# Kernel tuning notes

Hardware: AMD Instinct MI355X
Metric: run time of the kernel (lower is better)

## Reference

```python
import jax, jax.numpy as jnp
import numpy as np

B, S, E = 4, 2048, 2048
NH, NKV, HD = 16, 4, 128  # num_heads, num_kv_heads, head_dim
GROUP = NH // NKV


def setup_inputs() -> dict:
    key = jax.random.key(0)
    ks = jax.random.split(key, 6)
    sc = 0.02
    return {
        "hidden_states": jax.random.normal(ks[0], (B, S, E), dtype=jnp.float32),
        "q_w": jax.random.normal(ks[1], (E, NH * HD), dtype=jnp.float32) * sc,
        "k_w": jax.random.normal(ks[2], (E, NKV * HD), dtype=jnp.float32) * sc,
        "v_w": jax.random.normal(ks[3], (E, NKV * HD), dtype=jnp.float32) * sc,
        "out_w": jax.random.normal(ks[4], (NH * HD, E), dtype=jnp.float32) * sc,
        "out_b": jnp.zeros((E,), dtype=jnp.float32),
    }


def reference(hidden_states, q_w, k_w, v_w, out_w, out_b):
    x = hidden_states
    # projections (no bias on q/k/v, bias on out_proj)
    q = (x @ q_w).reshape(B, S, NH, HD).transpose(0, 2, 1, 3)    # [B,NH,S,HD]
    k = (x @ k_w).reshape(B, S, NKV, HD).transpose(0, 2, 1, 3)   # [B,NKV,S,HD]
    v = (x @ v_w).reshape(B, S, NKV, HD).transpose(0, 2, 1, 3)   # [B,NKV,S,HD]

    # GQA: each kv head serves GROUP consecutive query heads (matches loop order)
    k_exp = jnp.repeat(k, GROUP, axis=1)  # [B,NH,S,HD]
    v_exp = jnp.repeat(v, GROUP, axis=1)

    # GPT-Neo: fp32 attention, NO 1/sqrt(d) scaling
    qf = q.astype(jnp.float32)
    kf = k_exp.astype(jnp.float32)
    scores = jnp.einsum("bhqd,bhkd->bhqk", qf, kf)  # [B,NH,S,S]

    causal = jnp.tril(jnp.ones((S, S), dtype=bool))[None, None]
    mask_value = jnp.finfo(scores.dtype).min
    scores = jnp.where(causal, scores, mask_value)

    attn = jax.nn.softmax(scores, axis=-1).astype(v.dtype)
    ctx = jnp.einsum("bhqk,bhkd->bhqd", attn, v_exp)  # [B,NH,S,HD]

    out = ctx.transpose(0, 2, 1, 3).reshape(B, S, NH * HD)
    return out @ out_w + out_b
```

## Files before the change

kernel.cpp:

```cpp
#include <hip/hip_runtime.h>

typedef unsigned short u16;
typedef unsigned int   u32;
typedef __attribute__((ext_vector_type(8))) _Float16 f16x8;
typedef __attribute__((ext_vector_type(2))) __fp16   fp16x2;
typedef __attribute__((ext_vector_type(4))) float    f32x4;

#define LOG2E 1.44269504088896340f

__device__ __forceinline__ u16 f2h(float x) {
  union { _Float16 h; u16 u; } c;
  c.h = (_Float16)x;
  return c.u;
}
__device__ __forceinline__ u32 pk2(float a, float b) {
  union { fp16x2 h; u32 u; } c;
  c.h = __builtin_amdgcn_cvt_pkrtz(a, b);
  return c.u;
}
__device__ __forceinline__ void swap32(u32& a, u32& b) {
  asm volatile("v_permlane32_swap_b32 %0, %1" : "+v"(a), "+v"(b));
}
__device__ __forceinline__ void swap16(u32& a, u32& b) {
  asm volatile("v_permlane16_swap_b32 %0, %1" : "+v"(a), "+v"(b));
}
__device__ __forceinline__ void gload16(const u16* g, u16* l) {
  __builtin_amdgcn_global_load_lds(
      (const __attribute__((address_space(1))) void*)g,
      (__attribute__((address_space(3))) void*)l, 16, 0, 0);
}
__device__ __forceinline__ f32x4 MFMA(f16x8 a, f16x8 b, f32x4 c) {
  return __builtin_amdgcn_mfma_f32_16x16x32_f16(a, b, c, 0, 0, 0);
}

__global__ void conv_f16(const float4* __restrict__ src, u16* __restrict__ d, int n4) {
  int i = blockIdx.x * 256 + threadIdx.x;
  if (i >= n4) return;
  float4 v = src[i];
  union { u16 u[4]; uint2 q; } H;
  H.u[0] = f2h(v.x); H.u[1] = f2h(v.y); H.u[2] = f2h(v.z); H.u[3] = f2h(v.w);
  *(uint2*)&d[(size_t)i * 4] = H.q;
}

__global__ void transpose_f16(const float* __restrict__ src, int K, int N,
                              u16* __restrict__ d, int rowOff) {
  __shared__ float t[32][33];
  int n0 = blockIdx.x * 32, k0 = blockIdx.y * 32;
  int tx = threadIdx.x, ty = threadIdx.y;
#pragma unroll
  for (int i = 0; i < 4; ++i)
    t[ty + 8 * i][tx] = src[(size_t)(k0 + ty + 8 * i) * N + n0 + tx];
  __syncthreads();
#pragma unroll
  for (int i = 0; i < 4; ++i) {
    int n = n0 + ty + 8 * i, k = k0 + tx;
    d[(size_t)(rowOff + n) * 2048 + k] = f2h(t[tx][ty + 8 * i]);
  }
}

__global__ __launch_bounds__(512) void gemm_qkv(
    const u16* __restrict__ A, const u16* __restrict__ B,
    u16* __restrict__ Qf, u16* __restrict__ Kf, u16* __restrict__ VT) {
  const int K = 2048;
  const int NS = K / 32;
  __shared__ u16 As[3][256 * 32];
  __shared__ u16 Bs[3][128 * 32];
  int tid = threadIdx.x;
  int l = tid & 63, w = tid >> 6;
  int lr = l & 15, lg = l >> 4;
  int wr = w >> 1, wc = w & 1;
  int r0 = tid >> 2;
  int ssrc = (((tid & 3) ^ ((r0 >> 1) & 3))) * 8;
  size_t half = (size_t)128 * K;
  int swz = (lr >> 1) & 3;
  int aoff = (wr * 64 + lr) * 32 + (lg ^ swz) * 8;
  int boff = (wc * 64 + lr) * 32 + (lg ^ swz) * 8;

  for (int job = blockIdx.x; job < 768; job += 512) {
    int lidx = (job & 7) * 96 + (job >> 3);
    int bx = lidx % 24, by = lidx / 24;
    int rowA = by * 256, colB = bx * 128;
    const u16* ga = A + (size_t)(rowA + r0) * K + ssrc;
    const u16* gb = B + (size_t)(colB + r0) * K + ssrc;
    f32x4 acc[4][4] = {};

    gload16(ga, &As[0][tid * 8]);
    gload16(ga + half, &As[0][4096 + tid * 8]);
    gload16(gb, &Bs[0][tid * 8]);
    gload16(ga + 32, &As[1][tid * 8]);
    gload16(ga + 32 + half, &As[1][4096 + tid * 8]);
    gload16(gb + 32, &Bs[1][tid * 8]);
    asm volatile("s_waitcnt vmcnt(3)" ::: "memory");
    __builtin_amdgcn_sched_barrier(0);
    __builtin_amdgcn_s_barrier();
    __builtin_amdgcn_sched_barrier(0);

    for (int t = 0; t < NS; ++t) {
      int cur = t % 3, nxt = (t + 2) % 3;
      bool pre = (t + 2 < NS);
      int kb2 = (t + 2) * 32;
      f16x8 ah[4], bh[4];
#pragma unroll
      for (int i = 0; i < 4; ++i)
        ah[i] = *(const f16x8*)&As[cur][aoff + i * 512];
#pragma unroll
      for (int j = 0; j < 4; ++j)
        bh[j] = *(const f16x8*)&Bs[cur][boff + j * 512];
      if (pre) {
        gload16(ga + kb2, &As[nxt][tid * 8]);
        gload16(ga + kb2 + half, &As[nxt][4096 + tid * 8]);
        gload16(gb + kb2, &Bs[nxt][tid * 8]);
      }
      __builtin_amdgcn_s_setprio(1);
#pragma unroll
      for (int i = 0; i < 4; ++i)
#pragma unroll
        for (int j = 0; j < 4; ++j)
          acc[i][j] = MFMA(ah[i], bh[j], acc[i][j]);
      __builtin_amdgcn_s_setprio(0);
      if (pre) {
        asm volatile("s_waitcnt vmcnt(3)" ::: "memory");
      } else {
        asm volatile("s_waitcnt vmcnt(0)" ::: "memory");
      }
      __builtin_amdgcn_sched_barrier(0);
      __builtin_amdgcn_s_barrier();
      __builtin_amdgcn_sched_barrier(0);
    }

#pragma unroll
    for (int i = 0; i < 4; ++i) {
      int row0 = rowA + wr * 64 + i * 16 + lg * 4;
#pragma unroll
      for (int j = 0; j < 4; ++j) {
        int c = colB + wc * 64 + j * 16 + lr;
        f32x4 v = acc[i][j];
        if (c < 2048) {
#pragma unroll
          for (int r = 0; r < 4; ++r)
            Qf[(size_t)(row0 + r) * 2048 + c] = f2h(v[r]);
        } else if (c < 2560) {
          int ck = c - 2048;
#pragma unroll
          for (int r = 0; r < 4; ++r)
            Kf[(size_t)(row0 + r) * 512 + ck] = f2h(v[r]);
        } else {
          int cv = c - 2560, kvh = cv >> 7, d = cv & 127;
          int b = row0 >> 11, t2 = row0 & 2047;
          union { u16 u[4]; uint2 q; } P;
#pragma unroll
          for (int r = 0; r < 4; ++r) P.u[r] = f2h(v[r]);
          *(uint2*)&VT[((size_t)(b * 4 + kvh) * 128 + d) * 2048 + t2] = P.q;
        }
      }
    }
    __builtin_amdgcn_s_barrier();
    __builtin_amdgcn_sched_barrier(0);
  }
}

__global__ __launch_bounds__(512) void gemm_out(
    const u16* __restrict__ A, const u16* __restrict__ B,
    float* __restrict__ Out, const float* __restrict__ bias) {
  const int K = 2048;
  const int NS = K / 32;
  __shared__ u16 As[3][256 * 32];
  __shared__ u16 Bs[3][128 * 32];
  int tid = threadIdx.x;
  int l = tid & 63, w = tid >> 6;
  int lr = l & 15, lg = l >> 4;
  int wr = w >> 1, wc = w & 1;
  int p = blockIdx.x;
  int lidx = (p & 7) * 64 + (p >> 3);
  int bx = lidx & 15, by = lidx >> 4;
  int rowA = by * 256, colB = bx * 128;
  int r0 = tid >> 2;
  int ssrc = (((tid & 3) ^ ((r0 >> 1) & 3))) * 8;
  const u16* ga = A + (size_t)(rowA + r0) * K + ssrc;
  const u16* gb = B + (size_t)(colB + r0) * K + ssrc;
  size_t half = (size_t)128 * K;
  f32x4 acc[4][4] = {};
  int swz = (lr >> 1) & 3;
  int aoff = (wr * 64 + lr) * 32 + (lg ^ swz) * 8;
  int boff = (wc * 64 + lr) * 32 + (lg ^ swz) * 8;

  gload16(ga, &As[0][tid * 8]);
  gload16(ga + half, &As[0][4096 + tid * 8]);
  gload16(gb, &Bs[0][tid * 8]);
  gload16(ga + 32, &As[1][tid * 8]);
  gload16(ga + 32 + half, &As[1][4096 + tid * 8]);
  gload16(gb + 32, &Bs[1][tid * 8]);
  asm volatile("s_waitcnt vmcnt(3)" ::: "memory");
  __builtin_amdgcn_sched_barrier(0);
  __builtin_amdgcn_s_barrier();
  __builtin_amdgcn_sched_barrier(0);

  for (int t = 0; t < NS; ++t) {
    int cur = t % 3, nxt = (t + 2) % 3;
    bool pre = (t + 2 < NS);
    int kb2 = (t + 2) * 32;
    f16x8 ah[4], bh[4];
#pragma unroll
    for (int i = 0; i < 4; ++i)
      ah[i] = *(const f16x8*)&As[cur][aoff + i * 512];
#pragma unroll
    for (int j = 0; j < 4; ++j)
      bh[j] = *(const f16x8*)&Bs[cur][boff + j * 512];
    if (pre) {
      gload16(ga + kb2, &As[nxt][tid * 8]);
      gload16(ga + kb2 + half, &As[nxt][4096 + tid * 8]);
      gload16(gb + kb2, &Bs[nxt][tid * 8]);
    }
    __builtin_amdgcn_s_setprio(1);
#pragma unroll
    for (int i = 0; i < 4; ++i)
#pragma unroll
      for (int j = 0; j < 4; ++j)
        acc[i][j] = MFMA(ah[i], bh[j], acc[i][j]);
    __builtin_amdgcn_s_setprio(0);
    if (pre) {
      asm volatile("s_waitcnt vmcnt(3)" ::: "memory");
    } else {
      asm volatile("s_waitcnt vmcnt(0)" ::: "memory");
    }
    __builtin_amdgcn_sched_barrier(0);
    __builtin_amdgcn_s_barrier();
    __builtin_amdgcn_sched_barrier(0);
  }

#pragma unroll
  for (int i = 0; i < 4; ++i) {
    int row0 = rowA + wr * 64 + i * 16 + lg * 4;
#pragma unroll
    for (int j = 0; j < 4; ++j) {
      int c = colB + wc * 64 + j * 16 + lr;
      float bb = bias[c];
#pragma unroll
      for (int r = 0; r < 4; ++r)
        Out[(size_t)(row0 + r) * 2048 + c] = acc[i][j][r] + bb;
    }
  }
}

__global__ __launch_bounds__(512) void attn_kernel(
    const u16* __restrict__ Qf, const u16* __restrict__ Kf,
    const u16* __restrict__ VT, u16* __restrict__ Ch) {
  __shared__ u16 Ks[2][64 * 128];
  __shared__ u16 Vs[2][128 * 64];

  int tid = threadIdx.x;
  int w = tid >> 6, l = tid & 63;
  int lr = l & 15, lg = l >> 4;

  int p = blockIdx.x;
  int bid = (p & 7) * 64 + (p >> 3);
  int pair = bid & 7;
  int hg = (bid >> 3) & 3;
  int kvh = (bid >> 5) & 3;
  int b = bid >> 7;
  int h = kvh * 4 + hg;

  const u16* Kb = Kf + (size_t)(b * 2048) * 512 + kvh * 128;
  const u16* Vb = VT + (size_t)((b * 4 + kvh) * 128) * 2048;

  auto STAGE_K = [&](int t, int bufi) {
    int kv0 = t * 64;
#pragma unroll
    for (int pp = 0; pp < 2; ++pp) {
      int o16 = pp * 512 + tid;
      int krow = o16 >> 4;
      int kslot = ((o16 & 15) ^ (krow & 7)) * 8;
      gload16(Kb + (size_t)(kv0 + krow) * 512 + kslot, &Ks[bufi][o16 * 8]);
    }
  };
  auto STAGE_V = [&](int t, int bufi) {
    int kv0 = t * 64;
#pragma unroll
    for (int pp = 0; pp < 2; ++pp) {
      int o16 = pp * 512 + tid;
      int vrow = o16 >> 3;
      int vslot = ((o16 & 7) ^ (vrow & 7)) * 8;
      gload16(Vb + (size_t)vrow * 2048 + kv0 + vslot, &Vs[bufi][o16 * 8]);
    }
  };

  for (int pass = 0; pass < 2; ++pass) {
    int tIdx = pass == 0 ? (15 - pair) : pair;
    int q0 = tIdx * 128;
    int qr0 = q0 + w * 16;
    int nt = q0 / 64 + 2;

    size_t qbase = (size_t)(b * 2048 + qr0 + lr) * 2048 + h * 128 + lg * 8;
    f16x8 qf[4];
#pragma unroll
    for (int d = 0; d < 4; ++d)
      qf[d] = *(const f16x8*)(Qf + qbase + d * 32);

    f32x4 o[8] = {};
    float mrun = -3e38f;
    float lp = 0.f;

    STAGE_K(0, 0);
    STAGE_V(0, 0);
    asm volatile("s_waitcnt vmcnt(0)" ::: "memory");
    __builtin_amdgcn_sched_barrier(0);
    __builtin_amdgcn_s_barrier();
    __builtin_amdgcn_sched_barrier(0);

    int cur = 0;
    for (int t = 0; t < nt; ++t) {
      int kv0 = t * 64;
      bool more = (t + 1 < nt);
      if (more) {
        STAGE_K(t + 1, cur ^ 1);
        STAGE_V(t + 1, cur ^ 1);
      }
      bool compute = (kv0 <= qr0 + 15);

      if (compute) {
        f32x4 s[4] = {};
        __builtin_amdgcn_s_setprio(1);
#pragma unroll
        for (int d = 0; d < 4; ++d) {
#pragma unroll
          for (int n = 0; n < 4; ++n) {
            int row = n * 16 + lr;
            int sl = ((d * 4 + lg) ^ (row & 7)) * 8;
            f16x8 kf = *(const f16x8*)&Ks[cur][row * 128 + sl];
            s[n] = MFMA(kf, qf[d], s[n]);
          }
        }
        __builtin_amdgcn_s_setprio(0);
        if (kv0 + 63 > qr0) {
#pragma unroll
          for (int n = 0; n < 4; ++n)
#pragma unroll
            for (int r = 0; r < 4; ++r)
              if (kv0 + n * 16 + lg * 4 + r > qr0 + lr) s[n][r] = -3e38f;
        }
        float m0 = fmaxf(fmaxf(s[0][0], s[0][1]), fmaxf(s[0][2], s[0][3]));
        float m1 = fmaxf(fmaxf(s[1][0], s[1][1]), fmaxf(s[1][2], s[1][3]));
        float m2 = fmaxf(fmaxf(s[2][0], s[2][1]), fmaxf(s[2][2], s[2][3]));
        float m3 = fmaxf(fmaxf(s[3][0], s[3][1]), fmaxf(s[3][2], s[3][3]));
        float rowmax = fmaxf(fmaxf(m0, m1), fmaxf(m2, m3));
        if (__any(rowmax > mrun + 8.f)) {
          float tm = rowmax;
          tm = fmaxf(tm, __shfl_xor(tm, 16));
          tm = fmaxf(tm, __shfl_xor(tm, 32));
          float mn = fmaxf(mrun, tm);
          float alpha = __builtin_amdgcn_exp2f((mrun - mn) * LOG2E);
          mrun = mn;
          lp *= alpha;
#pragma unroll
          for (int dt = 0; dt < 8; ++dt)
#pragma unroll
            for (int r = 0; r < 4; ++r) o[dt][r] *= alpha;
        }
        float mL = mrun * LOG2E;
        float pv[4][4];
#pragma unroll
        for (int n = 0; n < 4; ++n)
#pragma unroll
          for (int r = 0; r < 4; ++r) {
            pv[n][r] = __builtin_amdgcn_exp2f(fmaf(s[n][r], LOG2E, -mL));
            lp += pv[n][r];
          }
        u32 A0[4], A1[4];
#pragma unroll
        for (int n = 0; n < 4; ++n) {
          A0[n] = pk2(pv[n][0], pv[n][1]);
          A1[n] = pk2(pv[n][2], pv[n][3]);
        }
        swap32(A0[0], A0[2]); swap32(A0[1], A0[3]);
        swap32(A1[0], A1[2]); swap32(A1[1], A1[3]);
        swap16(A0[0], A0[2]); swap16(A0[1], A0[3]);
        swap16(A1[0], A1[2]); swap16(A1[1], A1[3]);
        swap32(A0[0], A0[1]); swap32(A0[2], A0[3]);
        swap32(A1[0], A1[1]); swap32(A1[2], A1[3]);
        union { u32 w4[4]; f16x8 v; } P0, P1;
        P0.w4[0] = A0[0]; P0.w4[1] = A1[0]; P0.w4[2] = A0[2]; P0.w4[3] = A1[2];
        P1.w4[0] = A0[1]; P1.w4[1] = A1[1]; P1.w4[2] = A0[3]; P1.w4[3] = A1[3];
        __builtin_amdgcn_s_setprio(1);
#pragma unroll
        for (int n2 = 0; n2 < 2; ++n2) {
          f16x8 pf = n2 ? P1.v : P0.v;
#pragma unroll
          for (int dt = 0; dt < 8; ++dt) {
            int d = dt * 16 + lr;
            f16x8 vf = *(const f16x8*)&Vs[cur][d * 64 + (((n2 * 4 + lg) ^ (lr & 7)) * 8)];
            o[dt] = MFMA(vf, pf, o[dt]);
          }
        }
        __builtin_amdgcn_s_setprio(0);
      }
      asm volatile("s_waitcnt vmcnt(0) lgkmcnt(0)" ::: "memory");
      __builtin_amdgcn_sched_barrier(0);
      __builtin_amdgcn_s_barrier();
      __builtin_amdgcn_sched_barrier(0);
      cur ^= 1;
    }
    lp += __shfl_xor(lp, 16);
    lp += __shfl_xor(lp, 32);
    float inv = 1.0f / lp;
    size_t orow = (size_t)(b * 2048 + qr0 + lr) * 2048 + h * 128 + lg * 4;
#pragma unroll
    for (int dt = 0; dt < 8; ++dt) {
      uint2 pkt;
      pkt.x = pk2(o[dt][0] * inv, o[dt][1] * inv);
      pkt.y = pk2(o[dt][2] * inv, o[dt][3] * inv);
      *(uint2*)&Ch[orow + dt * 16] = pkt;
    }
  }
}

extern "C" void kernel_launch(void* const* d_in, const int* in_sizes, int n_in,
                              void* d_out, int out_size, void* d_ws, size_t ws_size,
                              hipStream_t stream) {
  const float* X  = (const float*)d_in[0];
  const float* qw = (const float*)d_in[1];
  const float* kw = (const float*)d_in[2];
  const float* vw = (const float*)d_in[3];
  const float* ow = (const float*)d_in[4];
  const float* ob = (const float*)d_in[5];
  float* Out = (float*)d_out;

  char* ws = (char*)d_ws;
  size_t off = 0;
  auto alloc = [&](size_t bytes) -> void* {
    void* p = ws + off;
    off += (bytes + 255) & ~(size_t)255;
    return p;
  };
  const size_t MK = (size_t)8192 * 2048;
  u16* Xf = (u16*)alloc(MK * 2);
  u16* Bt = (u16*)alloc((size_t)3072 * 2048 * 2);
  u16* OW = (u16*)alloc((size_t)2048 * 2048 * 2);
  u16* Qf = (u16*)alloc(MK * 2);
  u16* Kf = (u16*)alloc((size_t)8192 * 512 * 2);
  u16* VT = (u16*)alloc((size_t)8192 * 512 * 2);
  u16* Ch = (u16*)alloc(MK * 2);

  conv_f16<<<dim3(16384), dim3(256), 0, stream>>>((const float4*)X, Xf, (int)(MK / 4));
  dim3 tb(32, 8);
  transpose_f16<<<dim3(64, 64), tb, 0, stream>>>(qw, 2048, 2048, Bt, 0);
  transpose_f16<<<dim3(16, 64), tb, 0, stream>>>(kw, 2048, 512, Bt, 2048);
  transpose_f16<<<dim3(16, 64), tb, 0, stream>>>(vw, 2048, 512, Bt, 2560);
  transpose_f16<<<dim3(64, 64), tb, 0, stream>>>(ow, 2048, 2048, OW, 0);
  gemm_qkv<<<dim3(512), dim3(512), 0, stream>>>(Xf, Bt, Qf, Kf, VT);
  attn_kernel<<<dim3(512), dim3(512), 0, stream>>>(Qf, Kf, VT, Ch);
  gemm_out<<<dim3(512), dim3(512), 0, stream>>>(Ch, OW, Out, ob);
}
```

Baseline: 336.4 us.

## Retile output GEMM to 256x256 blocks with K=64 double-buffered interleaved staging

The output projection GEMM moves from 256x128 tiles with a 3-stage K=32 pipeline to 256x256 tiles with a 2-stage K=64 pipeline, and the grid shrinks from 512 to 256 blocks. Each warp now computes a 128x64 sub-tile, and global prefetches for A and B are interleaved between four MFMA phases separated by barriers. This raises arithmetic intensity and cuts LDS and global traffic per FLOP. In exchange, register pressure roughly doubles (128 accumulator floats per lane), there is only one block per CU on 256 CUs, and pipeline depth is shallower.

```diff
diff --git a/kernel.cpp b/kernel.cpp
--- a/kernel.cpp
+++ b/kernel.cpp
@@ -163,81 +163,134 @@
     const u16* __restrict__ A, const u16* __restrict__ B,
     float* __restrict__ Out, const float* __restrict__ bias) {
   const int K = 2048;
-  const int NS = K / 32;
-  __shared__ u16 As[3][256 * 32];
-  __shared__ u16 Bs[3][128 * 32];
+  const int NS = K / 64;
+  __shared__ u16 As[2][256 * 64];
+  __shared__ u16 Bs[2][256 * 64];
   int tid = threadIdx.x;
   int l = tid & 63, w = tid >> 6;
   int lr = l & 15, lg = l >> 4;
-  int wr = w >> 1, wc = w & 1;
+  int wm = w >> 2, wn = w & 3;
   int p = blockIdx.x;
-  int lidx = (p & 7) * 64 + (p >> 3);
-  int bx = lidx & 15, by = lidx >> 4;
-  int rowA = by * 256, colB = bx * 128;
-  int r0 = tid >> 2;
-  int ssrc = (((tid & 3) ^ ((r0 >> 1) & 3))) * 8;
-  const u16* ga = A + (size_t)(rowA + r0) * K + ssrc;
-  const u16* gb = B + (size_t)(colB + r0) * K + ssrc;
-  size_t half = (size_t)128 * K;
-  f32x4 acc[4][4] = {};
-  int swz = (lr >> 1) & 3;
-  int aoff = (wr * 64 + lr) * 32 + (lg ^ swz) * 8;
-  int boff = (wc * 64 + lr) * 32 + (lg ^ swz) * 8;
-
-  gload16(ga, &As[0][tid * 8]);
-  gload16(ga + half, &As[0][4096 + tid * 8]);
-  gload16(gb, &Bs[0][tid * 8]);
-  gload16(ga + 32, &As[1][tid * 8]);
-  gload16(ga + 32 + half, &As[1][4096 + tid * 8]);
-  gload16(gb + 32, &Bs[1][tid * 8]);
-  asm volatile("s_waitcnt vmcnt(3)" ::: "memory");
+  int lidx = (p & 7) * 32 + (p >> 3);
+  int bx = lidx & 7, by = lidx >> 3;
+  int rowA = by * 256, colB = bx * 256;
+  int srow = tid >> 3, sslot = tid & 7;
+  int soff = ((sslot ^ (srow & 7))) * 8;
+  const u16* ga = A + (size_t)(rowA + srow) * K + soff;
+  const u16* gb = B + (size_t)(colB + srow) * K + soff;
+  size_t sweep = (size_t)64 * K;
+  f32x4 acc[8][4] = {};
+
+  auto STAGE_A = [&](int kb, int bi) {
+#pragma unroll
+    for (int i = 0; i < 4; ++i)
+      gload16(ga + i * sweep + kb, &As[bi][i * 4096 + tid * 8]);
+  };
+  auto STAGE_B = [&](int kb, int bi) {
+#pragma unroll
+    for (int i = 0; i < 4; ++i)
+      gload16(gb + i * sweep + kb, &Bs[bi][i * 4096 + tid * 8]);
+  };
+
+  STAGE_A(0, 0);
+  STAGE_B(0, 0);
+  asm volatile("s_waitcnt vmcnt(0)" ::: "memory");
   __builtin_amdgcn_sched_barrier(0);
   __builtin_amdgcn_s_barrier();
   __builtin_amdgcn_sched_barrier(0);
 
   for (int t = 0; t < NS; ++t) {
-    int cur = t % 3, nxt = (t + 2) % 3;
-    bool pre = (t + 2 < NS);
-    int kb2 = (t + 2) * 32;
-    f16x8 ah[4], bh[4];
-#pragma unroll
-    for (int i = 0; i < 4; ++i)
-      ah[i] = *(const f16x8*)&As[cur][aoff + i * 512];
-#pragma unroll
-    for (int j = 0; j < 4; ++j)
-      bh[j] = *(const f16x8*)&Bs[cur][boff + j * 512];
-    if (pre) {
-      gload16(ga + kb2, &As[nxt][tid * 8]);
-      gload16(ga + kb2 + half, &As[nxt][4096 + tid * 8]);
-      gload16(gb + kb2, &Bs[nxt][tid * 8]);
-    }
+    int cur = t & 1, nxt = cur ^ 1;
+    bool pre = (t + 1 < NS);
+    int kb1 = (t + 1) * 64;
+    const u16* Ab = &As[cur][0];
+    const u16* Bb = &Bs[cur][0];
+    f16x8 afr[4][2], bfr[4][2];
+#pragma unroll
+    for (int mi = 0; mi < 4; ++mi)
+#pragma unroll
+      for (int kk = 0; kk < 2; ++kk) {
+        int row = wm * 128 + mi * 16 + lr;
+        afr[mi][kk] = *(const f16x8*)&Ab[row * 64 + (((kk * 4 + lg) ^ (row & 7)) * 8)];
+      }
+#pragma unroll
+    for (int nj = 0; nj < 2; ++nj)
+#pragma unroll
+      for (int kk = 0; kk < 2; ++kk) {
+        int row = wn * 64 + nj * 16 + lr;
+        bfr[nj][kk] = *(const f16x8*)&Bb[row * 64 + (((kk * 4 + lg) ^ (row & 7)) * 8)];
+      }
+    if (pre) STAGE_A(kb1, nxt);
     __builtin_amdgcn_s_setprio(1);
 #pragma unroll
-    for (int i = 0; i < 4; ++i)
-#pragma unroll
-      for (int j = 0; j < 4; ++j)
-        acc[i][j] = MFMA(ah[i], bh[j], acc[i][j]);
+    for (int mi = 0; mi < 4; ++mi)
+#pragma unroll
+      for (int nj = 0; nj < 2; ++nj) {
+        acc[mi][nj] = MFMA(afr[mi][0], bfr[nj][0], acc[mi][nj]);
+        acc[mi][nj] = MFMA(afr[mi][1], bfr[nj][1], acc[mi][nj]);
+      }
     __builtin_amdgcn_s_setprio(0);
-    if (pre) {
-      asm volatile("s_waitcnt vmcnt(3)" ::: "memory");
-    } else {
-      asm volatile("s_waitcnt vmcnt(0)" ::: "memory");
-    }
+    __builtin_amdgcn_s_barrier();
+#pragma unroll
+    for (int nj = 2; nj < 4; ++nj)
+#pragma unroll
+      for (int kk = 0; kk < 2; ++kk) {
+        int row = wn * 64 + nj * 16 + lr;
+        bfr[nj][kk] = *(const f16x8*)&Bb[row * 64 + (((kk * 4 + lg) ^ (row & 7)) * 8)];
+      }
+    if (pre) STAGE_B(kb1, nxt);
+    __builtin_amdgcn_s_setprio(1);
+#pragma unroll
+    for (int mi = 0; mi < 4; ++mi)
+#pragma unroll
+      for (int nj = 2; nj < 4; ++nj) {
+        acc[mi][nj] = MFMA(afr[mi][0], bfr[nj][0], acc[mi][nj]);
+        acc[mi][nj] = MFMA(afr[mi][1], bfr[nj][1], acc[mi][nj]);
+      }
+    __builtin_amdgcn_s_setprio(0);
+    __builtin_amdgcn_s_barrier();
+#pragma unroll
+    for (int mi = 0; mi < 4; ++mi)
+#pragma unroll
+      for (int kk = 0; kk < 2; ++kk) {
+        int row = wm * 128 + 64 + mi * 16 + lr;
+        afr[mi][kk] = *(const f16x8*)&Ab[row * 64 + (((kk * 4 + lg) ^ (row & 7)) * 8)];
+      }
+    __builtin_amdgcn_s_setprio(1);
+#pragma unroll
+    for (int mi = 0; mi < 4; ++mi)
+#pragma unroll
+      for (int nj = 0; nj < 2; ++nj) {
+        acc[4 + mi][nj] = MFMA(afr[mi][0], bfr[nj][0], acc[4 + mi][nj]);
+        acc[4 + mi][nj] = MFMA(afr[mi][1], bfr[nj][1], acc[4 + mi][nj]);
+      }
+    __builtin_amdgcn_s_setprio(0);
+    __builtin_amdgcn_s_barrier();
+    __builtin_amdgcn_s_setprio(1);
+#pragma unroll
+    for (int mi = 0; mi < 4; ++mi)
+#pragma unroll
+      for (int nj = 2; nj < 4; ++nj) {
+        acc[4 + mi][nj] = MFMA(afr[mi][0], bfr[nj][0], acc[4 + mi][nj]);
+        acc[4 + mi][nj] = MFMA(afr[mi][1], bfr[nj][1], acc[4 + mi][nj]);
+      }
+    __builtin_amdgcn_s_setprio(0);
+    asm volatile("s_waitcnt vmcnt(0)" ::: "memory");
     __builtin_amdgcn_sched_barrier(0);
     __builtin_amdgcn_s_barrier();
     __builtin_amdgcn_sched_barrier(0);
   }
 
 #pragma unroll
-  for (int i = 0; i < 4; ++i) {
-    int row0 = rowA + wr * 64 + i * 16 + lg * 4;
-#pragma unroll
-    for (int j = 0; j < 4; ++j) {
-      int c = colB + wc * 64 + j * 16 + lr;
+  for (int mi = 0; mi < 8; ++mi) {
+    int row0 = rowA + wm * 128 + mi * 16 + lg * 4;
+#pragma unroll
+    for (int nj = 0; nj < 4; ++nj) {
+      int c = colB + wn * 64 + nj * 16 + lr;
       float bb = bias[c];
 #pragma unroll
       for (int r = 0; r < 4; ++r)
-        Out[(size_t)(row0 + r) * 2048 + c] = acc[i][j][r] + bb;
+        Out[(size_t)(row0 + r) * 2048 + c] = acc[mi][nj][r] + bb;
     }
   }
 }
@@ -448,5 +501,5 @@
   transpose_f16<<<dim3(64, 64), tb, 0, stream>>>(ow, 2048, 2048, OW, 0);
   gemm_qkv<<<dim3(512), dim3(512), 0, stream>>>(Xf, Bt, Qf, Kf, VT);
   attn_kernel<<<dim3(512), dim3(512), 0, stream>>>(Qf, Kf, VT, Ch);
-  gemm_out<<<dim3(512), dim3(512), 0, stream>>>(Ch, OW, Out, ob);
-}
+  gemm_out<<<dim3(256), dim3(512), 0, stream>>>(Ch, OW, Out, ob);
+}
```

Result: faster. 323.7 us (median of 2 runs) (-3.8%).
